# Performance work log

Hardware: AMD Instinct MI355X
Metric: run time of the kernel (lower is better)

## Reference

```python
import jax, jax.numpy as jnp
import numpy as np
from jax.scipy.special import gammaln

N_NODES = 50000
N_EDGES = 1600000
IN_DIM, H1, H2 = 512, 256, 129  # H2 = hid_dims[-1] + 1 (kappa column)


def setup_inputs() -> dict:
    key = jax.random.key(0)
    k1, k2, k3, k4 = jax.random.split(key, 4)
    x = jax.random.normal(k1, (N_NODES, IN_DIM), dtype=jnp.float32)
    edge_index = jax.random.randint(k2, (2, N_EDGES), 0, N_NODES, dtype=jnp.int32)
    # Glorot-ish init for GCN weights
    W0 = jax.random.normal(k3, (IN_DIM, H1), dtype=jnp.float32) * (1.0 / np.sqrt(IN_DIM))
    W1 = jax.random.normal(k4, (H1, H2), dtype=jnp.float32) * (1.0 / np.sqrt(H1))
    return {"x": x, "edge_index": edge_index, "W0": W0, "W1": W1}


def _gcn_conv(h, W, src, dst, norm, n):
    # PyG GCNConv (bias=False): h' = D^-1/2 (A+I) D^-1/2 (h W)
    h = h @ W
    msg = h[src] * norm[:, None]          # [E+N, F_out]
    return jax.ops.segment_sum(msg, dst, num_segments=n)


def reference(x, edge_index, W0, W1):
    n = x.shape[0]
    loops = jnp.arange(n, dtype=edge_index.dtype)
    src = jnp.concatenate([edge_index[0], loops])
    dst = jnp.concatenate([edge_index[1], loops])
    # symmetric normalization with self-loops (deg >= 1, so rsqrt is safe)
    deg = jax.ops.segment_sum(jnp.ones_like(dst, dtype=x.dtype), dst, num_segments=n)
    dinv = jax.lax.rsqrt(deg)
    norm = dinv[src] * dinv[dst]          # [E+N]

    h = jax.nn.softplus(_gcn_conv(x, W0, src, dst, norm, n))
    # dropout is identity in eval mode (training=False)
    h = jax.nn.softplus(_gcn_conv(h, W1, src, dst, norm, n))

    lbd = h[:, :-1]                       # [N, 128] Weibull scale
    kappa = h[:, -1:] + 0.1               # [N, 1]   Weibull shape
    # deterministic (non-random-encoder / eval) reparameterization:
    # z = lbd * exp(lgamma(1 + 1/kappa))  == E[Weibull(lbd, kappa)]
    z = lbd * jnp.exp(gammaln(1.0 + 1.0 / kappa))
    return z, lbd, kappa
```

## Files before the change

kernel.cpp:

```cpp
#include <hip/hip_runtime.h>
#include <hip/hip_bf16.h>
#include <math.h>


typedef unsigned short ushort_t;
typedef __attribute__((ext_vector_type(8))) short bf16x8;
typedef __attribute__((ext_vector_type(4))) float f32x4;

__device__ __forceinline__ ushort_t f2bf(float f) {
    union { float f; unsigned u; } x; x.f = f;
    unsigned r = x.u + 0x7FFF + ((x.u >> 16) & 1);
    return (ushort_t)(r >> 16);
}
__device__ __forceinline__ float bf2f(ushort_t s) {
    union { unsigned u; float f; } x; x.u = ((unsigned)s) << 16; return x.f;
}

__device__ __forceinline__ void async_copy16(const void* gsrc, void* ldst) {
    __builtin_amdgcn_global_load_lds(
        (const __attribute__((address_space(1))) unsigned int*)gsrc,
        (__attribute__((address_space(3))) unsigned int*)ldst,
        16, 0, 0);
}


__global__ __launch_bounds__(256) void count_kernel(const int* __restrict__ dst,
                                                    int* __restrict__ cnt, int E)
{
    int e = blockIdx.x * blockDim.x + threadIdx.x;
    if (e < E) atomicAdd(&cnt[dst[e]], 1);
}

__global__ __launch_bounds__(1024) void scan_local(const int* __restrict__ cnt,
                                                   int* __restrict__ rowptr,
                                                   float* __restrict__ dinv,
                                                   int* __restrict__ blksum, int N)
{
    __shared__ int wsum[16];
    int tid = threadIdx.x, lane = tid & 63, wid = tid >> 6;
    int i = blockIdx.x * 1024 + tid;
    int v = (i < N) ? cnt[i] : 0;
    if (i < N) dinv[i] = rsqrtf((float)(v + 1));
    int s = v;
#pragma unroll
    for (int off = 1; off < 64; off <<= 1) {
        int t = __shfl_up(s, off, 64);
        if (lane >= off) s += t;
    }
    if (lane == 63) wsum[wid] = s;
    __syncthreads();
    if (tid < 16) {
        int w = wsum[tid];
#pragma unroll
        for (int off = 1; off < 16; off <<= 1) {
            int t = __shfl_up(w, off, 64);
            if (tid >= off) w += t;
        }
        wsum[tid] = w;
    }
    __syncthreads();
    int excl = s - v + (wid ? wsum[wid - 1] : 0);
    if (i < N) rowptr[i] = excl;
    if (tid == 0) blksum[blockIdx.x] = wsum[15];
}

__global__ __launch_bounds__(64) void scan_blk(const int* __restrict__ blksum,
                                               int* __restrict__ blkoff,
                                               int nblk, int* __restrict__ rowptr, int N)
{
    int tid = threadIdx.x;
    int v = (tid < nblk) ? blksum[tid] : 0;
    int s = v;
#pragma unroll
    for (int off = 1; off < 64; off <<= 1) {
        int t = __shfl_up(s, off, 64);
        if (tid >= off) s += t;
    }
    if (tid < nblk) blkoff[tid] = s - v;
    if (tid == nblk - 1) rowptr[N] = s;
}

__global__ __launch_bounds__(256) void scan_add(int* __restrict__ rowptr,
                                                int* __restrict__ cursor,
                                                const int* __restrict__ blkoff, int N)
{
    int i = blockIdx.x * blockDim.x + threadIdx.x;
    if (i < N) {
        int r = rowptr[i] + blkoff[i >> 10];
        rowptr[i] = r;
        cursor[i] = r;
    }
}

__global__ __launch_bounds__(256) void scatter_kernel(const int* __restrict__ src,
                                                      const int* __restrict__ dst,
                                                      int* __restrict__ cursor,
                                                      int* __restrict__ col, int E)
{
    int e = blockIdx.x * blockDim.x + threadIdx.x;
    if (e < E) {
        int d = dst[e];
        int pos = atomicAdd(&cursor[d], 1);
        col[pos] = src[e];
    }
}


__global__ __launch_bounds__(256) void conv_x(const float* __restrict__ x,
                                              ushort_t* __restrict__ Abig,
                                              int M, int M_pad)
{
    int id = blockIdx.x * blockDim.x + threadIdx.x;
    int r = id >> 7, q = id & 127;
    if (r >= M_pad) return;
    float4 v = make_float4(0.f, 0.f, 0.f, 0.f);
    if (r < M) v = *reinterpret_cast<const float4*>(&x[(size_t)r * 512 + q * 4]);
    ushort4 h, l;
    h.x = f2bf(v.x); l.x = f2bf(v.x - bf2f(h.x));
    h.y = f2bf(v.y); l.y = f2bf(v.y - bf2f(h.y));
    h.z = f2bf(v.z); l.z = f2bf(v.z - bf2f(h.z));
    h.w = f2bf(v.w); l.w = f2bf(v.w - bf2f(h.w));
    ushort_t* rowp = Abig + (size_t)r * 1024;
    *reinterpret_cast<ushort4*>(rowp + q * 4)       = h;
    *reinterpret_cast<ushort4*>(rowp + 512 + q * 4) = l;
}

__global__ __launch_bounds__(256) void conv_w0(const float* __restrict__ W0,
                                               ushort_t* __restrict__ BT)
{
    int id = blockIdx.x * blockDim.x + threadIdx.x;
    int k = id & 511, n = id >> 9;
    if (n >= 256) return;
    float v = W0[(size_t)k * 256 + n];
    ushort_t h = f2bf(v);
    ushort_t l = f2bf(v - bf2f(h));
    ushort_t* rowp = BT + (size_t)n * 1536;
    rowp[k] = h; rowp[512 + k] = h; rowp[1024 + k] = l;
}

__global__ __launch_bounds__(256) void conv_w1(const float* __restrict__ W1,
                                               ushort_t* __restrict__ BT,
                                               float* __restrict__ W1col)
{
    int id = blockIdx.x * blockDim.x + threadIdx.x;
    int k = id & 255, n = id >> 8;
    if (n >= 128) return;
    float v = W1[(size_t)k * 129 + n];
    ushort_t h = f2bf(v);
    ushort_t l = f2bf(v - bf2f(h));
    ushort_t* rowp = BT + (size_t)n * 768;
    rowp[k] = h; rowp[256 + k] = h; rowp[512 + k] = l;
    if (n == 0) W1col[k] = W1[(size_t)k * 129 + 128];
}

__global__ __launch_bounds__(256) void gemm_bf16(const ushort_t* __restrict__ A, int lda,
                                                 const ushort_t* __restrict__ BT, int ldbt,
                                                 float* __restrict__ C, int ldc,
                                                 int M, int K, int kwrap)
{
    __shared__ short As[128 * 32];
    __shared__ short Bs[128 * 32];

    int tid  = threadIdx.x;
    int w    = tid >> 6;
    int lane = tid & 63;
    int lm   = lane & 15;
    int lq   = lane >> 4;
    int bm   = blockIdx.x * 128;
    int bn   = blockIdx.y * 128;
    int wr   = (w >> 1) * 64;
    int wc   = (w & 1) * 64;

    f32x4 acc[4][4];
#pragma unroll
    for (int i = 0; i < 4; ++i)
#pragma unroll
        for (int j = 0; j < 4; ++j) acc[i][j] = (f32x4)(0.f);

    int srow = (lane >> 2);
    int scol = (lane & 3) * 16;

    for (int k0 = 0; k0 < K; k0 += 32) {
        int ka = (k0 < kwrap) ? k0 : (k0 - kwrap);
#pragma unroll
        for (int q = 0; q < 2; ++q) {
            int r = w * 32 + q * 16 + srow;
            const char* ga = (const char*)A + ((size_t)(bm + r) * lda + ka) * 2 + scol;
            async_copy16(ga, (char*)As + (size_t)(w * 32 + q * 16) * 64);
        }
#pragma unroll
        for (int q = 0; q < 2; ++q) {
            int r = w * 32 + q * 16 + srow;
            const char* gb = (const char*)BT + ((size_t)(bn + r) * ldbt + k0) * 2 + scol;
            async_copy16(gb, (char*)Bs + (size_t)(w * 32 + q * 16) * 64);
        }
        __syncthreads();

        bf16x8 afr[4], bfr[4];
#pragma unroll
        for (int mi = 0; mi < 4; ++mi)
            afr[mi] = *reinterpret_cast<const bf16x8*>(&As[(wr + mi * 16 + lm) * 32 + lq * 8]);
#pragma unroll
        for (int ni = 0; ni < 4; ++ni)
            bfr[ni] = *reinterpret_cast<const bf16x8*>(&Bs[(wc + ni * 16 + lm) * 32 + lq * 8]);
#pragma unroll
        for (int mi = 0; mi < 4; ++mi)
#pragma unroll
            for (int ni = 0; ni < 4; ++ni)
                acc[mi][ni] = __builtin_amdgcn_mfma_f32_16x16x32_bf16(
                    afr[mi], bfr[ni], acc[mi][ni], 0, 0, 0);
        __syncthreads();
    }

#pragma unroll
    for (int mi = 0; mi < 4; ++mi) {
#pragma unroll
        for (int ni = 0; ni < 4; ++ni) {
            int rbase = bm + wr + mi * 16 + lq * 4;
            int cc    = bn + wc + ni * 16 + lm;
#pragma unroll
            for (int e = 0; e < 4; ++e) {
                int r = rbase + e;
                if (r < M) C[(size_t)r * ldc + cc] = acc[mi][ni][e];
            }
        }
    }
}


__device__ __forceinline__ float softplus_f(float x)
{
    return fmaxf(x, 0.f) + log1pf(expf(-fabsf(x)));
}

__device__ __forceinline__ void fma4(float4& a, float w, const float4& v)
{
    a.x = fmaf(w, v.x, a.x);
    a.y = fmaf(w, v.y, a.y);
    a.z = fmaf(w, v.z, a.z);
    a.w = fmaf(w, v.w, a.w);
}

__device__ __forceinline__ void fma2(float2& a, float w, const float2& v)
{
    a.x = fmaf(w, v.x, a.x);
    a.y = fmaf(w, v.y, a.y);
}

__global__ __launch_bounds__(256) void agg1_kernel(const float* __restrict__ T1,
                                                   const float* __restrict__ dinv,
                                                   const int* __restrict__ rowptr,
                                                   const int* __restrict__ col,
                                                   const float* __restrict__ W1col,
                                                   ushort_t* __restrict__ H1big,
                                                   float* __restrict__ T2k, int N)
{
    int node = blockIdx.x * 4 + (threadIdx.x >> 6);
    if (node >= N) return;
    int lane = threadIdx.x & 63;
    float di = dinv[node];
    int beg = rowptr[node], end = rowptr[node + 1];

    float4 a0 = make_float4(0.f, 0.f, 0.f, 0.f);
    float4 a1 = a0, a2 = a0, a3 = a0;

    int e = beg;
    for (; e + 4 <= end; e += 4) {
        int s0 = col[e], s1 = col[e + 1], s2 = col[e + 2], s3 = col[e + 3];
        float w0 = dinv[s0], w1 = dinv[s1], w2 = dinv[s2], w3 = dinv[s3];
        float4 v0 = *reinterpret_cast<const float4*>(&T1[(size_t)s0 * 256 + lane * 4]);
        float4 v1 = *reinterpret_cast<const float4*>(&T1[(size_t)s1 * 256 + lane * 4]);
        float4 v2 = *reinterpret_cast<const float4*>(&T1[(size_t)s2 * 256 + lane * 4]);
        float4 v3 = *reinterpret_cast<const float4*>(&T1[(size_t)s3 * 256 + lane * 4]);
        fma4(a0, w0, v0); fma4(a1, w1, v1); fma4(a2, w2, v2); fma4(a3, w3, v3);
    }
    for (; e < end; ++e) {
        int s = col[e];
        float w = dinv[s];
        float4 v = *reinterpret_cast<const float4*>(&T1[(size_t)s * 256 + lane * 4]);
        fma4(a0, w, v);
    }

    float4 self = *reinterpret_cast<const float4*>(&T1[(size_t)node * 256 + lane * 4]);
    float4 o;
    o.x = softplus_f((a0.x + a1.x + a2.x + a3.x + self.x * di) * di);
    o.y = softplus_f((a0.y + a1.y + a2.y + a3.y + self.y * di) * di);
    o.z = softplus_f((a0.z + a1.z + a2.z + a3.z + self.z * di) * di);
    o.w = softplus_f((a0.w + a1.w + a2.w + a3.w + self.w * di) * di);

    ushort4 h, l;
    h.x = f2bf(o.x); l.x = f2bf(o.x - bf2f(h.x));
    h.y = f2bf(o.y); l.y = f2bf(o.y - bf2f(h.y));
    h.z = f2bf(o.z); l.z = f2bf(o.z - bf2f(h.z));
    h.w = f2bf(o.w); l.w = f2bf(o.w - bf2f(h.w));
    ushort_t* rowp = H1big + (size_t)node * 512;
    *reinterpret_cast<ushort4*>(rowp + lane * 4)       = h;
    *reinterpret_cast<ushort4*>(rowp + 256 + lane * 4) = l;

    float4 wv = *reinterpret_cast<const float4*>(&W1col[lane * 4]);
    float tk = o.x * wv.x + o.y * wv.y + o.z * wv.z + o.w * wv.w;
#pragma unroll
    for (int off = 32; off > 0; off >>= 1)
        tk += __shfl_down(tk, off, 64);
    if (lane == 0) T2k[node] = tk;
}

__global__ __launch_bounds__(256) void agg2_kernel(const float* __restrict__ T2,
                                                   const float* __restrict__ T2k,
                                                   const float* __restrict__ dinv,
                                                   const int* __restrict__ rowptr,
                                                   const int* __restrict__ col,
                                                   float* __restrict__ z_out,
                                                   float* __restrict__ lbd_out,
                                                   float* __restrict__ kap_out, int N)
{
    int node = blockIdx.x * 4 + (threadIdx.x >> 6);
    if (node >= N) return;
    int lane = threadIdx.x & 63;
    float di = dinv[node];
    int beg = rowptr[node], end = rowptr[node + 1];

    float2 a0 = make_float2(0.f, 0.f);
    float2 a1 = a0, a2 = a0, a3 = a0;
    float k0 = 0.f, k1 = 0.f, k2 = 0.f, k3 = 0.f;

    int e = beg;
    for (; e + 4 <= end; e += 4) {
        int s0 = col[e], s1 = col[e + 1], s2 = col[e + 2], s3 = col[e + 3];
        float w0 = dinv[s0], w1 = dinv[s1], w2 = dinv[s2], w3 = dinv[s3];
        k0 = fmaf(w0, T2k[s0], k0);
        k1 = fmaf(w1, T2k[s1], k1);
        k2 = fmaf(w2, T2k[s2], k2);
        k3 = fmaf(w3, T2k[s3], k3);
        float2 v0 = *reinterpret_cast<const float2*>(&T2[(size_t)s0 * 128 + lane * 2]);
        float2 v1 = *reinterpret_cast<const float2*>(&T2[(size_t)s1 * 128 + lane * 2]);
        float2 v2 = *reinterpret_cast<const float2*>(&T2[(size_t)s2 * 128 + lane * 2]);
        float2 v3 = *reinterpret_cast<const float2*>(&T2[(size_t)s3 * 128 + lane * 2]);
        fma2(a0, w0, v0); fma2(a1, w1, v1); fma2(a2, w2, v2); fma2(a3, w3, v3);
    }
    for (; e < end; ++e) {
        int s = col[e];
        float w = dinv[s];
        k0 = fmaf(w, T2k[s], k0);
        float2 v = *reinterpret_cast<const float2*>(&T2[(size_t)s * 128 + lane * 2]);
        fma2(a0, w, v);
    }

    float2 self = *reinterpret_cast<const float2*>(&T2[(size_t)node * 128 + lane * 2]);
    float2 sp;
    sp.x = softplus_f((a0.x + a1.x + a2.x + a3.x + self.x * di) * di);
    sp.y = softplus_f((a0.y + a1.y + a2.y + a3.y + self.y * di) * di);

    float ak = ((k0 + k1 + k2 + k3) + T2k[node] * di) * di;
    float kv = softplus_f(ak) + 0.1f;
    float g  = expf(lgammaf(1.0f + 1.0f / kv));
    if (lane == 0) kap_out[node] = kv;

    size_t o = (size_t)node * 128 + lane * 2;
    float2 zv = make_float2(sp.x * g, sp.y * g);
    *reinterpret_cast<float2*>(&lbd_out[o]) = sp;
    *reinterpret_cast<float2*>(&z_out[o])   = zv;
}

extern "C" void kernel_launch(void* const* d_in, const int* in_sizes, int n_in,
                              void* d_out, int out_size, void* d_ws, size_t ws_size,
                              hipStream_t stream)
{
    const float* x  = (const float*)d_in[0];
    const int*   ei = (const int*)d_in[1];
    const float* W0 = (const float*)d_in[2];
    const float* W1 = (const float*)d_in[3];

    const int N = in_sizes[0] / 512;
    const int E = in_sizes[1] / 2;
    const int* src = ei;
    const int* dst = ei + E;

    const int mblocks = (N + 127) / 128;
    const int M_pad   = mblocks * 128;
    const int nchunk  = (N + 1023) / 1024;

    char* w = (char*)d_ws;
    size_t off = 0;
    auto take = [&](size_t bytes) -> void* {
        void* p = (void*)(w + off);
        off = (off + bytes + 255) & ~(size_t)255;
        return p;
    };
    int*      cnt    = (int*)take((size_t)N * 4);
    int*      rowptr = (int*)take((size_t)(N + 1) * 4);
    int*      cursor = (int*)take((size_t)N * 4);
    float*    dinv   = (float*)take((size_t)N * 4);
    int*      col    = (int*)take((size_t)E * 4);
    int*      blksum = (int*)take(64 * 4);
    int*      blkoff = (int*)take(64 * 4);
    ushort_t* W0bigT = (ushort_t*)take((size_t)256 * 1536 * 2);
    ushort_t* W1bigT = (ushort_t*)take((size_t)128 * 768 * 2);
    float*    W1col  = (float*)take((size_t)256 * 4);
    float*    T2k    = (float*)take((size_t)N * 4);
    float*    T1     = (float*)take((size_t)N * 256 * 4);
    float*    T2     = T1;
    ushort_t* Abig   = (ushort_t*)take((size_t)M_pad * 1024 * 2);
    ushort_t* H1big  = Abig;

    float* z_out   = (float*)d_out;
    float* lbd_out = z_out + (size_t)N * 128;
    float* kap_out = lbd_out + (size_t)N * 128;

    hipMemsetAsync(cnt, 0, (size_t)N * 4, stream);
    count_kernel<<<(E + 255) / 256, 256, 0, stream>>>(dst, cnt, E);
    scan_local<<<nchunk, 1024, 0, stream>>>(cnt, rowptr, dinv, blksum, N);
    scan_blk<<<1, 64, 0, stream>>>(blksum, blkoff, nchunk, rowptr, N);
    scan_add<<<(N + 255) / 256, 256, 0, stream>>>(rowptr, cursor, blkoff, N);
    scatter_kernel<<<(E + 255) / 256, 256, 0, stream>>>(src, dst, cursor, col, E);

    conv_x<<<(M_pad * 128) / 256, 256, 0, stream>>>(x, Abig, N, M_pad);
    conv_w0<<<(256 * 512) / 256, 256, 0, stream>>>(W0, W0bigT);
    conv_w1<<<(128 * 256) / 256, 256, 0, stream>>>(W1, W1bigT, W1col);

    dim3 g1(mblocks, 2);
    gemm_bf16<<<g1, 256, 0, stream>>>(Abig, 1024, W0bigT, 1536, T1, 256, N, 1536, 1024);

    agg1_kernel<<<(N + 3) / 4, 256, 0, stream>>>(T1, dinv, rowptr, col, W1col, H1big, T2k, N);

    dim3 g2(mblocks, 1);
    gemm_bf16<<<g2, 256, 0, stream>>>(H1big, 512, W1bigT, 768, T2, 128, N, 768, 512);

    agg2_kernel<<<(N + 3) / 4, 256, 0, stream>>>(T2, T2k, dinv, rowptr, col,
                                                 z_out, lbd_out, kap_out, N);
}
```

Measured before the change: 820.6 us.

## Bucket CSR edges by source range and aggregate in lockstep source-bucket phases

Builds a two-level CSR keyed by (destination, source bucket of 2048 nodes). A larger multi-level scan produces it, with degrees derived from the bucket row pointers. The aggregation kernels now give each wave 8 destination nodes and walk all nodes bucket by bucket with block barriers between phases. The goal is to keep the gathered feature rows of concurrently processed sources in L2 cache instead of doing fully random gathers. In exchange there are more preprocessing kernels and a much larger count array, T1 is reused as scratch, and the per-wave serial loops over 8 nodes reduce memory-level parallelism and add 25 barriers.

```diff
diff --git a/kernel.cpp b/kernel.cpp
--- a/kernel.cpp
+++ b/kernel.cpp
@@ -6,6 +6,9 @@
 typedef unsigned short ushort_t;
 typedef __attribute__((ext_vector_type(8))) short bf16x8;
 typedef __attribute__((ext_vector_type(4))) float f32x4;
+
+#define NB 25
+#define BSHIFT 11
 
 __device__ __forceinline__ ushort_t f2bf(float f) {
     union { float f; unsigned u; } x; x.f = f;
@@ -24,23 +27,22 @@
 }
 
 
-__global__ __launch_bounds__(256) void count_kernel(const int* __restrict__ dst,
-                                                    int* __restrict__ cnt, int E)
+__global__ __launch_bounds__(256) void count2_kernel(const int* __restrict__ src,
+                                                     const int* __restrict__ dst,
+                                                     int* __restrict__ cnt2, int E)
 {
     int e = blockIdx.x * blockDim.x + threadIdx.x;
-    if (e < E) atomicAdd(&cnt[dst[e]], 1);
+    if (e < E) atomicAdd(&cnt2[dst[e] * NB + (src[e] >> BSHIFT)], 1);
 }
 
 __global__ __launch_bounds__(1024) void scan_local(const int* __restrict__ cnt,
-                                                   int* __restrict__ rowptr,
-                                                   float* __restrict__ dinv,
+                                                   int* __restrict__ outp,
                                                    int* __restrict__ blksum, int N)
 {
     __shared__ int wsum[16];
     int tid = threadIdx.x, lane = tid & 63, wid = tid >> 6;
     int i = blockIdx.x * 1024 + tid;
     int v = (i < N) ? cnt[i] : 0;
-    if (i < N) dinv[i] = rsqrtf((float)(v + 1));
     int s = v;
 #pragma unroll
     for (int off = 1; off < 64; off <<= 1) {
@@ -60,13 +62,13 @@
     }
     __syncthreads();
     int excl = s - v + (wid ? wsum[wid - 1] : 0);
-    if (i < N) rowptr[i] = excl;
+    if (i < N) outp[i] = excl;
     if (tid == 0) blksum[blockIdx.x] = wsum[15];
 }
 
 __global__ __launch_bounds__(64) void scan_blk(const int* __restrict__ blksum,
                                                int* __restrict__ blkoff,
-                                               int nblk, int* __restrict__ rowptr, int N)
+                                               int nblk, int* __restrict__ endp, int LEN)
 {
     int tid = threadIdx.x;
     int v = (tid < nblk) ? blksum[tid] : 0;
@@ -77,31 +79,43 @@
         if (tid >= off) s += t;
     }
     if (tid < nblk) blkoff[tid] = s - v;
-    if (tid == nblk - 1) rowptr[N] = s;
-}
-
-__global__ __launch_bounds__(256) void scan_add(int* __restrict__ rowptr,
-                                                int* __restrict__ cursor,
-                                                const int* __restrict__ blkoff, int N)
+    if (tid == nblk - 1) endp[LEN] = s;
+}
+
+__global__ __launch_bounds__(256) void final_add(int* __restrict__ R2,
+                                                 int* __restrict__ cursor2,
+                                                 const int* __restrict__ bs1p,
+                                                 const int* __restrict__ bo2, int LEN)
+{
+    int i = blockIdx.x * blockDim.x + threadIdx.x;
+    if (i < LEN) {
+        int r = R2[i] + bs1p[i >> 10] + bo2[i >> 20];
+        R2[i] = r;
+        cursor2[i] = r;
+    }
+}
+
+__global__ __launch_bounds__(256) void dinv_kernel(const int* __restrict__ R2,
+                                                   float* __restrict__ dinv, int N)
 {
     int i = blockIdx.x * blockDim.x + threadIdx.x;
     if (i < N) {
-        int r = rowptr[i] + blkoff[i >> 10];
-        rowptr[i] = r;
-        cursor[i] = r;
-    }
-}
-
-__global__ __launch_bounds__(256) void scatter_kernel(const int* __restrict__ src,
-                                                      const int* __restrict__ dst,
-                                                      int* __restrict__ cursor,
-                                                      int* __restrict__ col, int E)
+        int beg = R2[i * NB];
+        int end = R2[(i + 1) * NB];
+        dinv[i] = rsqrtf((float)(end - beg + 1));
+    }
+}
+
+__global__ __launch_bounds__(256) void scatter2_kernel(const int* __restrict__ src,
+                                                       const int* __restrict__ dst,
+                                                       int* __restrict__ cursor2,
+                                                       int* __restrict__ col, int E)
 {
     int e = blockIdx.x * blockDim.x + threadIdx.x;
     if (e < E) {
-        int d = dst[e];
-        int pos = atomicAdd(&cursor[d], 1);
-        col[pos] = src[e];
+        int d = dst[e], s = src[e];
+        int pos = atomicAdd(&cursor2[d * NB + (s >> BSHIFT)], 1);
+        col[pos] = s;
     }
 }
 
@@ -249,117 +263,143 @@
 
 __global__ __launch_bounds__(256) void agg1_kernel(const float* __restrict__ T1,
                                                    const float* __restrict__ dinv,
-                                                   const int* __restrict__ rowptr,
+                                                   const int* __restrict__ R2,
                                                    const int* __restrict__ col,
                                                    const float* __restrict__ W1col,
                                                    ushort_t* __restrict__ H1big,
                                                    float* __restrict__ T2k, int N)
 {
-    int node = blockIdx.x * 4 + (threadIdx.x >> 6);
-    if (node >= N) return;
-    int lane = threadIdx.x & 63;
-    float di = dinv[node];
-    int beg = rowptr[node], end = rowptr[node + 1];
-
-    float4 a0 = make_float4(0.f, 0.f, 0.f, 0.f);
-    float4 a1 = a0, a2 = a0, a3 = a0;
-
-    int e = beg;
-    for (; e + 4 <= end; e += 4) {
-        int s0 = col[e], s1 = col[e + 1], s2 = col[e + 2], s3 = col[e + 3];
-        float w0 = dinv[s0], w1 = dinv[s1], w2 = dinv[s2], w3 = dinv[s3];
-        float4 v0 = *reinterpret_cast<const float4*>(&T1[(size_t)s0 * 256 + lane * 4]);
-        float4 v1 = *reinterpret_cast<const float4*>(&T1[(size_t)s1 * 256 + lane * 4]);
-        float4 v2 = *reinterpret_cast<const float4*>(&T1[(size_t)s2 * 256 + lane * 4]);
-        float4 v3 = *reinterpret_cast<const float4*>(&T1[(size_t)s3 * 256 + lane * 4]);
-        fma4(a0, w0, v0); fma4(a1, w1, v1); fma4(a2, w2, v2); fma4(a3, w3, v3);
-    }
-    for (; e < end; ++e) {
-        int s = col[e];
-        float w = dinv[s];
-        float4 v = *reinterpret_cast<const float4*>(&T1[(size_t)s * 256 + lane * 4]);
-        fma4(a0, w, v);
-    }
-
-    float4 self = *reinterpret_cast<const float4*>(&T1[(size_t)node * 256 + lane * 4]);
-    float4 o;
-    o.x = softplus_f((a0.x + a1.x + a2.x + a3.x + self.x * di) * di);
-    o.y = softplus_f((a0.y + a1.y + a2.y + a3.y + self.y * di) * di);
-    o.z = softplus_f((a0.z + a1.z + a2.z + a3.z + self.z * di) * di);
-    o.w = softplus_f((a0.w + a1.w + a2.w + a3.w + self.w * di) * di);
-
-    ushort4 h, l;
-    h.x = f2bf(o.x); l.x = f2bf(o.x - bf2f(h.x));
-    h.y = f2bf(o.y); l.y = f2bf(o.y - bf2f(h.y));
-    h.z = f2bf(o.z); l.z = f2bf(o.z - bf2f(h.z));
-    h.w = f2bf(o.w); l.w = f2bf(o.w - bf2f(h.w));
-    ushort_t* rowp = H1big + (size_t)node * 512;
-    *reinterpret_cast<ushort4*>(rowp + lane * 4)       = h;
-    *reinterpret_cast<ushort4*>(rowp + 256 + lane * 4) = l;
-
-    float4 wv = *reinterpret_cast<const float4*>(&W1col[lane * 4]);
-    float tk = o.x * wv.x + o.y * wv.y + o.z * wv.z + o.w * wv.w;
-#pragma unroll
-    for (int off = 32; off > 0; off >>= 1)
-        tk += __shfl_down(tk, off, 64);
-    if (lane == 0) T2k[node] = tk;
+    int wslot = __builtin_amdgcn_readfirstlane(threadIdx.x >> 6);
+    int lane  = threadIdx.x & 63;
+    int nbase = blockIdx.x * 32 + wslot * 8;
+
+    float4 acc[8];
+#pragma unroll
+    for (int q = 0; q < 8; ++q) acc[q] = make_float4(0.f, 0.f, 0.f, 0.f);
+
+    int bcur[8];
+#pragma unroll
+    for (int q = 0; q < 8; ++q) {
+        int node = nbase + q;
+        bcur[q] = (node < N) ? R2[node * NB] : 0;
+    }
+
+    const float* Trow = T1 + (size_t)lane * 4;
+
+    for (int p = 0; p < NB; ++p) {
+#pragma unroll
+        for (int q = 0; q < 8; ++q) {
+            int node = nbase + q;
+            if (node < N) {
+                int en = R2[node * NB + p + 1];
+                for (int e = bcur[q]; e < en; ++e) {
+                    int s   = col[e];
+                    float w = dinv[s];
+                    float4 v = *reinterpret_cast<const float4*>(Trow + (size_t)s * 256);
+                    fma4(acc[q], w, v);
+                }
+                bcur[q] = en;
+            }
+        }
+        __syncthreads();
+    }
+
+#pragma unroll
+    for (int q = 0; q < 8; ++q) {
+        int node = nbase + q;
+        if (node >= N) continue;
+        float di = dinv[node];
+        float4 self = *reinterpret_cast<const float4*>(Trow + (size_t)node * 256);
+        float4 o;
+        o.x = softplus_f((acc[q].x + self.x * di) * di);
+        o.y = softplus_f((acc[q].y + self.y * di) * di);
+        o.z = softplus_f((acc[q].z + self.z * di) * di);
+        o.w = softplus_f((acc[q].w + self.w * di) * di);
+
+        ushort4 h, l;
+        h.x = f2bf(o.x); l.x = f2bf(o.x - bf2f(h.x));
+        h.y = f2bf(o.y); l.y = f2bf(o.y - bf2f(h.y));
+        h.z = f2bf(o.z); l.z = f2bf(o.z - bf2f(h.z));
+        h.w = f2bf(o.w); l.w = f2bf(o.w - bf2f(h.w));
+        ushort_t* rowp = H1big + (size_t)node * 512;
+        *reinterpret_cast<ushort4*>(rowp + lane * 4)       = h;
+        *reinterpret_cast<ushort4*>(rowp + 256 + lane * 4) = l;
+
+        float4 wv = *reinterpret_cast<const float4*>(&W1col[lane * 4]);
+        float tk = o.x * wv.x + o.y * wv.y + o.z * wv.z + o.w * wv.w;
+#pragma unroll
+        for (int off = 32; off > 0; off >>= 1)
+            tk += __shfl_down(tk, off, 64);
+        if (lane == 0) T2k[node] = tk;
+    }
 }
 
 __global__ __launch_bounds__(256) void agg2_kernel(const float* __restrict__ T2,
                                                    const float* __restrict__ T2k,
                                                    const float* __restrict__ dinv,
-                                                   const int* __restrict__ rowptr,
+                                                   const int* __restrict__ R2,
                                                    const int* __restrict__ col,
                                                    float* __restrict__ z_out,
                                                    float* __restrict__ lbd_out,
                                                    float* __restrict__ kap_out, int N)
 {
-    int node = blockIdx.x * 4 + (threadIdx.x >> 6);
-    if (node >= N) return;
-    int lane = threadIdx.x & 63;
-    float di = dinv[node];
-    int beg = rowptr[node], end = rowptr[node + 1];
-
-    float2 a0 = make_float2(0.f, 0.f);
-    float2 a1 = a0, a2 = a0, a3 = a0;
-    float k0 = 0.f, k1 = 0.f, k2 = 0.f, k3 = 0.f;
-
-    int e = beg;
-    for (; e + 4 <= end; e += 4) {
-        int s0 = col[e], s1 = col[e + 1], s2 = col[e + 2], s3 = col[e + 3];
-        float w0 = dinv[s0], w1 = dinv[s1], w2 = dinv[s2], w3 = dinv[s3];
-        k0 = fmaf(w0, T2k[s0], k0);
-        k1 = fmaf(w1, T2k[s1], k1);
-        k2 = fmaf(w2, T2k[s2], k2);
-        k3 = fmaf(w3, T2k[s3], k3);
-        float2 v0 = *reinterpret_cast<const float2*>(&T2[(size_t)s0 * 128 + lane * 2]);
-        float2 v1 = *reinterpret_cast<const float2*>(&T2[(size_t)s1 * 128 + lane * 2]);
-        float2 v2 = *reinterpret_cast<const float2*>(&T2[(size_t)s2 * 128 + lane * 2]);
-        float2 v3 = *reinterpret_cast<const float2*>(&T2[(size_t)s3 * 128 + lane * 2]);
-        fma2(a0, w0, v0); fma2(a1, w1, v1); fma2(a2, w2, v2); fma2(a3, w3, v3);
-    }
-    for (; e < end; ++e) {
-        int s = col[e];
-        float w = dinv[s];
-        k0 = fmaf(w, T2k[s], k0);
-        float2 v = *reinterpret_cast<const float2*>(&T2[(size_t)s * 128 + lane * 2]);
-        fma2(a0, w, v);
-    }
-
-    float2 self = *reinterpret_cast<const float2*>(&T2[(size_t)node * 128 + lane * 2]);
-    float2 sp;
-    sp.x = softplus_f((a0.x + a1.x + a2.x + a3.x + self.x * di) * di);
-    sp.y = softplus_f((a0.y + a1.y + a2.y + a3.y + self.y * di) * di);
-
-    float ak = ((k0 + k1 + k2 + k3) + T2k[node] * di) * di;
-    float kv = softplus_f(ak) + 0.1f;
-    float g  = expf(lgammaf(1.0f + 1.0f / kv));
-    if (lane == 0) kap_out[node] = kv;
-
-    size_t o = (size_t)node * 128 + lane * 2;
-    float2 zv = make_float2(sp.x * g, sp.y * g);
-    *reinterpret_cast<float2*>(&lbd_out[o]) = sp;
-    *reinterpret_cast<float2*>(&z_out[o])   = zv;
+    int wslot = __builtin_amdgcn_readfirstlane(threadIdx.x >> 6);
+    int lane  = threadIdx.x & 63;
+    int nbase = blockIdx.x * 32 + wslot * 8;
+
+    float2 acc[8];
+    float  kk[8];
+#pragma unroll
+    for (int q = 0; q < 8; ++q) { acc[q] = make_float2(0.f, 0.f); kk[q] = 0.f; }
+
+    int bcur[8];
+#pragma unroll
+    for (int q = 0; q < 8; ++q) {
+        int node = nbase + q;
+        bcur[q] = (node < N) ? R2[node * NB] : 0;
+    }
+
+    const float* Trow = T2 + (size_t)lane * 2;
+
+    for (int p = 0; p < NB; ++p) {
+#pragma unroll
+        for (int q = 0; q < 8; ++q) {
+            int node = nbase + q;
+            if (node < N) {
+                int en = R2[node * NB + p + 1];
+                for (int e = bcur[q]; e < en; ++e) {
+                    int s   = col[e];
+                    float w = dinv[s];
+                    kk[q] = fmaf(w, T2k[s], kk[q]);
+                    float2 v = *reinterpret_cast<const float2*>(Trow + (size_t)s * 128);
+                    fma2(acc[q], w, v);
+                }
+                bcur[q] = en;
+            }
+        }
+        __syncthreads();
+    }
+
+#pragma unroll
+    for (int q = 0; q < 8; ++q) {
+        int node = nbase + q;
+        if (node >= N) continue;
+        float di = dinv[node];
+        float2 self = *reinterpret_cast<const float2*>(Trow + (size_t)node * 128);
+        float2 sp;
+        sp.x = softplus_f((acc[q].x + self.x * di) * di);
+        sp.y = softplus_f((acc[q].y + self.y * di) * di);
+
+        float ak = (kk[q] + T2k[node] * di) * di;
+        float kv = softplus_f(ak) + 0.1f;
+        float g  = expf(lgammaf(1.0f + 1.0f / kv));
+        if (lane == 0) kap_out[node] = kv;
+
+        size_t o = (size_t)node * 128 + lane * 2;
+        float2 zv = make_float2(sp.x * g, sp.y * g);
+        *reinterpret_cast<float2*>(&lbd_out[o]) = sp;
+        *reinterpret_cast<float2*>(&z_out[o])   = zv;
+    }
 }
 
 extern "C" void kernel_launch(void* const* d_in, const int* in_sizes, int n_in,
@@ -378,7 +418,9 @@
 
     const int mblocks = (N + 127) / 128;
     const int M_pad   = mblocks * 128;
-    const int nchunk  = (N + 1023) / 1024;
+    const int LEN     = N * NB;
+    const int nblk1   = (LEN + 1023) / 1024;
+    const int nblk2   = (nblk1 + 1023) / 1024;
 
     char* w = (char*)d_ws;
     size_t off = 0;
@@ -387,13 +429,13 @@
         off = (off + bytes + 255) & ~(size_t)255;
         return p;
     };
-    int*      cnt    = (int*)take((size_t)N * 4);
-    int*      rowptr = (int*)take((size_t)(N + 1) * 4);
-    int*      cursor = (int*)take((size_t)N * 4);
+    int*      R2     = (int*)take((size_t)(LEN + 1) * 4);
     float*    dinv   = (float*)take((size_t)N * 4);
     int*      col    = (int*)take((size_t)E * 4);
-    int*      blksum = (int*)take(64 * 4);
-    int*      blkoff = (int*)take(64 * 4);
+    int*      bs1    = (int*)take((size_t)1280 * 4);
+    int*      bs1p   = (int*)take((size_t)1280 * 4);
+    int*      bs2    = (int*)take((size_t)64 * 4);
+    int*      bo2    = (int*)take((size_t)64 * 4);
     ushort_t* W0bigT = (ushort_t*)take((size_t)256 * 1536 * 2);
     ushort_t* W1bigT = (ushort_t*)take((size_t)128 * 768 * 2);
     float*    W1col  = (float*)take((size_t)256 * 4);
@@ -403,16 +445,21 @@
     ushort_t* Abig   = (ushort_t*)take((size_t)M_pad * 1024 * 2);
     ushort_t* H1big  = Abig;
 
+    int* cnt2    = (int*)T1;
+    int* cursor2 = (int*)((char*)T1 + (size_t)16 * 1024 * 1024);
+
     float* z_out   = (float*)d_out;
     float* lbd_out = z_out + (size_t)N * 128;
     float* kap_out = lbd_out + (size_t)N * 128;
 
-    hipMemsetAsync(cnt, 0, (size_t)N * 4, stream);
-    count_kernel<<<(E + 255) / 256, 256, 0, stream>>>(dst, cnt, E);
-    scan_local<<<nchunk, 1024, 0, stream>>>(cnt, rowptr, dinv, blksum, N);
-    scan_blk<<<1, 64, 0, stream>>>(blksum, blkoff, nchunk, rowptr, N);
-    scan_add<<<(N + 255) / 256, 256, 0, stream>>>(rowptr, cursor, blkoff, N);
-    scatter_kernel<<<(E + 255) / 256, 256, 0, stream>>>(src, dst, cursor, col, E);
+    hipMemsetAsync(cnt2, 0, (size_t)LEN * 4, stream);
+    count2_kernel<<<(E + 255) / 256, 256, 0, stream>>>(src, dst, cnt2, E);
+    scan_local<<<nblk1, 1024, 0, stream>>>(cnt2, R2, bs1, LEN);
+    scan_local<<<nblk2, 1024, 0, stream>>>(bs1, bs1p, bs2, nblk1);
+    scan_blk<<<1, 64, 0, stream>>>(bs2, bo2, nblk2, R2, LEN);
+    final_add<<<(LEN + 255) / 256, 256, 0, stream>>>(R2, cursor2, bs1p, bo2, LEN);
+    dinv_kernel<<<(N + 255) / 256, 256, 0, stream>>>(R2, dinv, N);
+    scatter2_kernel<<<(E + 255) / 256, 256, 0, stream>>>(src, dst, cursor2, col, E);
 
     conv_x<<<(M_pad * 128) / 256, 256, 0, stream>>>(x, Abig, N, M_pad);
     conv_w0<<<(256 * 512) / 256, 256, 0, stream>>>(W0, W0bigT);
@@ -421,11 +468,11 @@
     dim3 g1(mblocks, 2);
     gemm_bf16<<<g1, 256, 0, stream>>>(Abig, 1024, W0bigT, 1536, T1, 256, N, 1536, 1024);
 
-    agg1_kernel<<<(N + 3) / 4, 256, 0, stream>>>(T1, dinv, rowptr, col, W1col, H1big, T2k, N);
+    agg1_kernel<<<(N + 31) / 32, 256, 0, stream>>>(T1, dinv, R2, col, W1col, H1big, T2k, N);
 
     dim3 g2(mblocks, 1);
     gemm_bf16<<<g2, 256, 0, stream>>>(H1big, 512, W1bigT, 768, T2, 128, N, 768, 512);
 
-    agg2_kernel<<<(N + 3) / 4, 256, 0, stream>>>(T2, T2k, dinv, rowptr, col,
-                                                 z_out, lbd_out, kap_out, N);
-}
+    agg2_kernel<<<(N + 31) / 32, 256, 0, stream>>>(T2, T2k, dinv, R2, col,
+                                                   z_out, lbd_out, kap_out, N);
+}
```

New measurement: 1.080 ms. 31.6% more time.
